# Kernel tuning notes

Measured on AMD Instinct MI355X. Metric: run time of the kernel, lower is better.

Reference implementation:

```python
import jax, jax.numpy as jnp
import numpy as np

# Dimensions (see shape_source)
D = 12       # tree depth / number of levels
N = 32768    # nodes per level
L = 3        # label_size
K = 4        # nary (max children)
HID = 128    # hidden_size == dim_E == dim_rep
V = 50000    # word_vocab_size
LAYERS = 2   # stacked NaryTreeLSTM layers


def setup_inputs() -> dict:
    key = jax.random.key(0)
    ks = jax.random.split(key, 10)
    s = 0.02  # weight init scale
    tokens = jax.random.randint(ks[0], (D, N, L), 0, V)
    # child indices in [-1, N]; -1 = no child, 0 = zero init row, 1..N = prev-level node
    indices = jax.random.randint(ks[1], (D, N, K), 0, N + 2) - 1
    E = jax.random.normal(ks[2], (V, HID))  # torch.randn init
    lin_w = jax.random.normal(ks[3], (HID, L * HID)) * s
    lin_b = jnp.zeros((HID,), jnp.float32)
    Uf_w = jax.random.normal(ks[4], (LAYERS, K * HID, K * HID)) * s
    Uf_b = jnp.zeros((LAYERS, K * HID), jnp.float32)
    Uiuo_w = jax.random.normal(ks[5], (LAYERS, 3 * HID, K * HID)) * s
    Uiuo_b = jnp.zeros((LAYERS, 3 * HID), jnp.float32)
    W_w = jax.random.normal(ks[6], (LAYERS, 4 * HID, HID)) * s
    W_b = jnp.zeros((LAYERS, 4 * HID), jnp.float32)
    return dict(tokens=tokens, indices=indices, E=E, lin_w=lin_w, lin_b=lin_b,
                Uf_w=Uf_w, Uf_b=Uf_b, Uiuo_w=Uiuo_w, Uiuo_b=Uiuo_b, W_w=W_w, W_b=W_b)


def _tree_lstm_layer(x, indices, Uf_w, Uf_b, Uiuo_w, Uiuo_b, W_w, W_b):
    """x: [D,N,HID], indices: [D,N,K] in [-1,N]. Returns (hs, cs): [D,N,HID]."""
    d = HID

    def step(carry, inp):
        h_full, c_full = carry              # [1+N, d]; row 0 is the zero init state
        xl, idx = inp                       # [N, d], [N, K]
        mask = (idx != -1)
        safe = jnp.where(mask, idx, 0)
        h = h_full[safe]                    # [N, K, d] gather of child hidden states
        c = c_full[safe]                    # [N, K, d]
        m = mask.astype(xl.dtype)[..., None]
        Wx = xl @ W_w.T + W_b               # [N, 4d]
        Wf, Wi, Wu, Wo = Wx[:, :d], Wx[:, d:2 * d], Wx[:, 2 * d:3 * d], Wx[:, 3 * d:]
        h_flat = h.reshape(N, K * d)
        fk = jax.nn.sigmoid(Wf[:, None, :] + (h_flat @ Uf_w.T + Uf_b).reshape(N, K, d))
        f = jnp.sum(fk * c * m, axis=1)     # masked sum over children
        iuo = h_flat @ Uiuo_w.T + Uiuo_b    # [N, 3d]
        i = jax.nn.sigmoid(iuo[:, :d] + Wi)
        u = jnp.tanh(iuo[:, d:2 * d] + Wu)
        o = jax.nn.sigmoid(iuo[:, 2 * d:] + Wo)
        new_c = i * u + f
        new_h = o * jnp.tanh(new_c)
        zero = jnp.zeros((1, d), xl.dtype)
        new_carry = (jnp.concatenate([zero, new_h], 0), jnp.concatenate([zero, new_c], 0))
        return new_carry, (new_h, new_c)

    init = (jnp.zeros((1 + N, d), x.dtype), jnp.zeros((1 + N, d), x.dtype))
    _, (hs, cs) = jax.lax.scan(step, init, (x, indices))
    return hs, cs


def reference(tokens, indices, E, lin_w, lin_b, Uf_w, Uf_b, Uiuo_w, Uiuo_b, W_w, W_b):
    # TreeEmbeddingLayer: gather token embeddings, concat label slots, project to HID
    emb = E[tokens].reshape(D, N, L * HID) @ lin_w.T + lin_b  # [D, N, HID]
    t = emb
    cs = None
    for l in range(LAYERS):
        skip = t
        hs, cs = _tree_lstm_layer(t, indices, Uf_w[l], Uf_b[l], Uiuo_w[l], Uiuo_b[l], W_w[l], W_b[l])
        t = hs + skip  # residual over levels
    hx = jnp.tile(t[-1][None], (2, 1, 1))   # [2, N, HID]
    cx = jnp.tile(cs[-1][None], (2, 1, 1))  # [2, N, HID]
    return hx, cx
```

## Files before the change

### kernel.cpp

```cpp
#include <hip/hip_runtime.h>
#include <cstdint>
#include <cstddef>

#define DD 12
#define NNODE 32768
#define LTOK 3
#define KCH 4
#define HD 128
#define NC_STEP 896
#define KD_STEP 640
#define NC_EMB 128
#define KD_EMB 384

typedef unsigned short u16;
typedef __attribute__((ext_vector_type(8))) __bf16 bf16x8;
typedef __attribute__((ext_vector_type(4))) float f32x4;

__device__ __forceinline__ float bf2f(unsigned int u) {
  union { unsigned int i; float f; } v; v.i = (u & 0xffffu) << 16; return v.f;
}
__device__ __forceinline__ u16 f2bf(float f) {
  union { float f; unsigned int i; } v; v.f = f;
  unsigned int x = v.i;
  return (u16)((x + 0x7fffu + ((x >> 16) & 1u)) >> 16);
}
__device__ __forceinline__ float sigm(float x) { return 1.f / (1.f + __expf(-x)); }
__device__ __forceinline__ float tanh_fast(float x) { return 1.f - 2.f / (1.f + __expf(2.f * x)); }
__device__ __forceinline__ void async16(const void* g, void* l) {
  __builtin_amdgcn_global_load_lds((const __attribute__((address_space(1))) unsigned int*)g,
                                   (__attribute__((address_space(3))) unsigned int*)l, 16, 0, 0);
}

#define BM 256
#define BN 128
#define BK 32

__global__ __launch_bounds__(512, 4) void gemm8_k(
    const u16* __restrict__ Abf, const u16* __restrict__ Tbf,
    const int* __restrict__ gidx, const u16* __restrict__ B,
    const float* __restrict__ bias, u16* __restrict__ outb,
    const u16* __restrict__ zbuf)
{
  __shared__ u16 As[3][BM * BK];
  __shared__ u16 Bs[3][BN * BK];
  const int t = threadIdx.x;
  const int w = t >> 6;
  const int L = t & 63;
  const int q = L >> 4;
  const int r16 = L >> 2;
  const int sub = L & 3;
  const int swz = sub ^ ((L >> 3) & 3);

  const int bid = blockIdx.x;
  const int wg = (bid & 7) * 112 + (bid >> 3);
  const int rt = wg / 7;
  const int ct = wg - rt * 7;
  const int row0 = rt * BM;
  const int col0 = ct * BN;

  const int wm = w >> 1;
  const int wn = w & 1;
  const int mrow = wm * 64;
  const int ncol = wn * 64;

  f32x4 acc[4][4];
#pragma unroll
  for (int a = 0; a < 4; ++a)
#pragma unroll
    for (int b = 0; b < 4; ++b)
      acc[a][b] = f32x4{0.f, 0.f, 0.f, 0.f};

  int4 cidx[2];
#pragma unroll
  for (int j = 0; j < 2; ++j)
    cidx[j] = *(const int4*)&gidx[(row0 + w * 32 + j * 16 + r16) * KCH];

  auto stageAll = [&](const int k0, const int sel) {
#pragma unroll
    for (int j = 0; j < 2; ++j) {
      const int rbase = w * 32 + j * 16;
      const u16* src;
      if (k0 < 4 * HD) {
        const int id = ((const int*)&cidx[j])[k0 >> 7];
        const u16* base = (id >= 1) ? (Abf + (size_t)(id - 1) * HD) : zbuf;
        src = base + (k0 & 127) + swz * 8;
      } else {
        src = Tbf + (size_t)(row0 + rbase + r16) * HD + (k0 - 4 * HD) + swz * 8;
      }
      async16(src, &As[sel][rbase * BK]);
    }
    const int rb = w * 16;
    async16(B + (size_t)(col0 + rb + r16) * KD_STEP + k0 + swz * 8,
            &Bs[sel][rb * BK]);
  };

  stageAll(0, 0);
  stageAll(32, 1);
  asm volatile("s_waitcnt vmcnt(3)" ::: "memory");
  __builtin_amdgcn_sched_barrier(0);
  __builtin_amdgcn_s_barrier();
  __builtin_amdgcn_sched_barrier(0);

  constexpr int NT = KD_STEP / BK;
#pragma unroll
  for (int tt = 0; tt < NT; ++tt) {
    const int rd = tt % 3;
    if (tt + 2 < NT) stageAll((tt + 2) * BK, (tt + 2) % 3);

    const int pc = (q ^ ((L >> 1) & 3)) * 8;
    bf16x8 af[4], bfv[4];
#pragma unroll
    for (int mt = 0; mt < 4; ++mt)
      af[mt] = *(const bf16x8*)&As[rd][(mrow + mt * 16 + (L & 15)) * BK + pc];
#pragma unroll
    for (int nt = 0; nt < 4; ++nt)
      bfv[nt] = *(const bf16x8*)&Bs[rd][(ncol + nt * 16 + (L & 15)) * BK + pc];

    __builtin_amdgcn_s_setprio(1);
#pragma unroll
    for (int mt = 0; mt < 4; ++mt)
#pragma unroll
      for (int nt = 0; nt < 4; ++nt)
        acc[mt][nt] = __builtin_amdgcn_mfma_f32_16x16x32_bf16(
            af[mt], bfv[nt], acc[mt][nt], 0, 0, 0);
    __builtin_amdgcn_s_setprio(0);

    if (tt < NT - 1) {
      if (tt + 2 < NT) asm volatile("s_waitcnt vmcnt(3)" ::: "memory");
      else             asm volatile("s_waitcnt vmcnt(0)" ::: "memory");
      __builtin_amdgcn_sched_barrier(0);
      __builtin_amdgcn_s_barrier();
      __builtin_amdgcn_sched_barrier(0);
    }
  }

#pragma unroll
  for (int nt = 0; nt < 4; ++nt) {
    const int col = col0 + ncol + nt * 16 + (L & 15);
    const float bb = bias[col];
#pragma unroll
    for (int mt = 0; mt < 4; ++mt) {
#pragma unroll
      for (int i = 0; i < 4; ++i) {
        const int row = row0 + mrow + mt * 16 + q * 4 + i;
        outb[(size_t)row * NC_STEP + col] = f2bf(acc[mt][nt][i] + bb);
      }
    }
  }
}

__global__ __launch_bounds__(256, 4) void gemm_emb_k(
    const u16* __restrict__ Ebf, const int* __restrict__ tokd,
    const u16* __restrict__ Lbf, const float* __restrict__ bias,
    float* __restrict__ outf, u16* __restrict__ outb)
{
  __shared__ u16 As[3][64 * BK];
  __shared__ u16 Bs[3][128 * BK];
  const int t = threadIdx.x;
  const int w = t >> 6;
  const int L = t & 63;
  const int q = L >> 4;
  const int r16 = L >> 2;
  const int sub = L & 3;
  const int swz = sub ^ ((L >> 3) & 3);
  const int row0 = blockIdx.x * 64;

  const int wm = w >> 1;
  const int wn = w & 1;
  const int mrow = wm * 32;
  const int ncol = wn * 64;

  f32x4 acc[2][4];
#pragma unroll
  for (int a = 0; a < 2; ++a)
#pragma unroll
    for (int b = 0; b < 4; ++b)
      acc[a][b] = f32x4{0.f, 0.f, 0.f, 0.f};

  const int arow = row0 + w * 16 + r16;
  int tok[3];
#pragma unroll
  for (int j = 0; j < 3; ++j)
    tok[j] = tokd[arow * LTOK + j];

  auto stageAll = [&](const int k0, const int sel) {
    const int id = tok[k0 >> 7];
    async16(Ebf + (size_t)id * HD + (k0 & 127) + swz * 8,
            &As[sel][(w * 16) * BK]);
#pragma unroll
    for (int j = 0; j < 2; ++j) {
      const int rb = w * 32 + j * 16;
      async16(Lbf + (size_t)(rb + r16) * KD_EMB + k0 + swz * 8,
              &Bs[sel][rb * BK]);
    }
  };

  stageAll(0, 0);
  stageAll(32, 1);
  asm volatile("s_waitcnt vmcnt(3)" ::: "memory");
  __builtin_amdgcn_sched_barrier(0);
  __builtin_amdgcn_s_barrier();
  __builtin_amdgcn_sched_barrier(0);

  constexpr int NT = KD_EMB / BK;
#pragma unroll
  for (int tt = 0; tt < NT; ++tt) {
    const int rd = tt % 3;
    if (tt + 2 < NT) stageAll((tt + 2) * BK, (tt + 2) % 3);

    const int pc = (q ^ ((L >> 1) & 3)) * 8;
    bf16x8 af[2], bfv[4];
#pragma unroll
    for (int mt = 0; mt < 2; ++mt)
      af[mt] = *(const bf16x8*)&As[rd][(mrow + mt * 16 + (L & 15)) * BK + pc];
#pragma unroll
    for (int nt = 0; nt < 4; ++nt)
      bfv[nt] = *(const bf16x8*)&Bs[rd][(ncol + nt * 16 + (L & 15)) * BK + pc];

    __builtin_amdgcn_s_setprio(1);
#pragma unroll
    for (int mt = 0; mt < 2; ++mt)
#pragma unroll
      for (int nt = 0; nt < 4; ++nt)
        acc[mt][nt] = __builtin_amdgcn_mfma_f32_16x16x32_bf16(
            af[mt], bfv[nt], acc[mt][nt], 0, 0, 0);
    __builtin_amdgcn_s_setprio(0);

    if (tt < NT - 1) {
      if (tt + 2 < NT) asm volatile("s_waitcnt vmcnt(3)" ::: "memory");
      else             asm volatile("s_waitcnt vmcnt(0)" ::: "memory");
      __builtin_amdgcn_sched_barrier(0);
      __builtin_amdgcn_s_barrier();
      __builtin_amdgcn_sched_barrier(0);
    }
  }

#pragma unroll
  for (int nt = 0; nt < 4; ++nt) {
    const int col = ncol + nt * 16 + (L & 15);
    const float bb = bias[col];
#pragma unroll
    for (int mt = 0; mt < 2; ++mt) {
#pragma unroll
      for (int i = 0; i < 4; ++i) {
        const int row = row0 + mrow + mt * 16 + q * 4 + i;
        const float v = acc[mt][nt][i] + bb;
        outf[(size_t)row * NC_EMB + col] = v;
        outb[(size_t)row * NC_EMB + col] = f2bf(v);
      }
    }
  }
}

__global__ __launch_bounds__(256) void cell_k(
    const u16* __restrict__ pre, const int* __restrict__ idxs,
    const float* __restrict__ c_prev, float* __restrict__ c_cur,
    u16* __restrict__ h_cur, float* __restrict__ t_io, u16* __restrict__ tbf)
{
  const int g = blockIdx.x * 256 + threadIdx.x;
  const int r = g >> 7;
  const int j = g & 127;
  const u16* pr = pre + (size_t)r * NC_STEP;
  float f = 0.f;
#pragma unroll
  for (int k = 0; k < KCH; ++k) {
    const int id = idxs[r * KCH + k];
    const float cg = (id >= 1) ? c_prev[(size_t)(id - 1) * HD + j] : 0.f;
    f += sigm(bf2f(pr[k * HD + j])) * cg;
  }
  const float iv = sigm(bf2f(pr[4 * HD + j]));
  const float uv = tanh_fast(bf2f(pr[5 * HD + j]));
  const float ov = sigm(bf2f(pr[6 * HD + j]));
  const float cn = iv * uv + f;
  const float hv = ov * tanh_fast(cn);
  c_cur[g] = cn;
  h_cur[g] = f2bf(hv);
  const float tn = t_io[g] + hv;
  t_io[g] = tn;
  tbf[g] = f2bf(tn);
}

__global__ __launch_bounds__(256) void conv_k(const float* __restrict__ src,
                                              u16* __restrict__ dst, int n4)
{
  const int g = blockIdx.x * 256 + threadIdx.x;
  if (g < n4) {
    float4 v = ((const float4*)src)[g];
    ((ushort4*)dst)[g] = make_ushort4(f2bf(v.x), f2bf(v.y), f2bf(v.z), f2bf(v.w));
  }
}

__global__ __launch_bounds__(256) void prep_k(
    const float* __restrict__ Uf_w, const float* __restrict__ Uf_b,
    const float* __restrict__ Uiuo_w, const float* __restrict__ Uiuo_b,
    const float* __restrict__ W_w, const float* __restrict__ W_b,
    u16* __restrict__ Ubig, float* __restrict__ biasbig)
{
  const int l = blockIdx.y;
  const int e = blockIdx.x * 256 + threadIdx.x;
  const int c = e / KD_STEP;
  const int k = e % KD_STEP;
  float v;
  if (k < 512) {
    v = (c < 512) ? Uf_w[((size_t)l * 512 + c) * 512 + k]
                  : Uiuo_w[((size_t)l * 384 + (c - 512)) * 512 + k];
  } else {
    const int q = k - 512;
    const int wr = (c < 512) ? (c & 127) : (128 + (c - 512));
    v = W_w[((size_t)l * 512 + wr) * 128 + q];
  }
  Ubig[((size_t)l * 896 + c) * 640 + k] = f2bf(v);
  if (e < 896) {
    const float b = (e < 512)
        ? (Uf_b[l * 512 + e] + W_b[l * 512 + (e & 127)])
        : (Uiuo_b[l * 384 + (e - 512)] + W_b[l * 512 + 128 + (e - 512)]);
    biasbig[l * 896 + e] = b;
  }
}

__global__ __launch_bounds__(256) void fin_k(
    const float* __restrict__ t_fin, const float* __restrict__ c_fin,
    float* __restrict__ out)
{
  const size_t NH = (size_t)NNODE * HD;
  const size_t g = (size_t)blockIdx.x * 256 + threadIdx.x;
  const float h = t_fin[g];
  const float c = c_fin[g];
  out[g] = h;
  out[NH + g] = h;
  out[2 * NH + g] = c;
  out[3 * NH + g] = c;
}

extern "C" void kernel_launch(void* const* d_in, const int* in_sizes, int n_in,
                              void* d_out, int out_size, void* d_ws, size_t ws_size,
                              hipStream_t stream)
{
  (void)in_sizes; (void)n_in; (void)out_size; (void)ws_size;
  const int*   tokens  = (const int*)d_in[0];
  const int*   indices = (const int*)d_in[1];
  const float* E       = (const float*)d_in[2];
  const float* lin_w   = (const float*)d_in[3];
  const float* lin_b   = (const float*)d_in[4];
  const float* Uf_w    = (const float*)d_in[5];
  const float* Uf_b    = (const float*)d_in[6];
  const float* Uiuo_w  = (const float*)d_in[7];
  const float* Uiuo_b  = (const float*)d_in[8];
  const float* W_w     = (const float*)d_in[9];
  const float* W_b     = (const float*)d_in[10];
  float* out = (float*)d_out;

  const size_t NH = (size_t)NNODE * HD;

  char* ws = (char*)d_ws;
  size_t off = 0;
  auto alloc = [&](size_t bytes) -> void* {
    void* p = ws + off;
    off = (off + bytes + 255) & ~(size_t)255;
    return p;
  };
  u16*   Ubig    = (u16*)alloc((size_t)2 * 896 * 640 * 2);
  float* biasbig = (float*)alloc(2 * 896 * 4);
  u16*   Ebf     = (u16*)alloc((size_t)50000 * HD * 2);
  u16*   Lbf     = (u16*)alloc((size_t)HD * KD_EMB * 2);
  float* tslice  = (float*)alloc(NH * 4);
  u16*   tbf     = (u16*)alloc(NH * 2);
  u16*   h0a     = (u16*)alloc(NH * 2);
  u16*   h0b     = (u16*)alloc(NH * 2);
  u16*   h1a     = (u16*)alloc(NH * 2);
  u16*   h1b     = (u16*)alloc(NH * 2);
  float* c0a     = (float*)alloc(NH * 4);
  float* c0b     = (float*)alloc(NH * 4);
  float* c1a     = (float*)alloc(NH * 4);
  float* c1b     = (float*)alloc(NH * 4);
  u16*   pre     = (u16*)alloc((size_t)NNODE * NC_STEP * 2);
  u16*   zbuf    = (u16*)alloc(512);

  u16*   h0[2] = {h0a, h0b};
  u16*   h1[2] = {h1a, h1b};
  float* c0[2] = {c0a, c0b};
  float* c1[2] = {c1a, c1b};

  hipMemsetAsync(zbuf, 0, 512, stream);
  hipMemsetAsync(h0[0], 0, NH * 2, stream);
  hipMemsetAsync(h1[0], 0, NH * 2, stream);
  hipMemsetAsync(c0[0], 0, NH * 4, stream);
  hipMemsetAsync(c1[0], 0, NH * 4, stream);
  prep_k<<<dim3(2240, 2), 256, 0, stream>>>(Uf_w, Uf_b, Uiuo_w, Uiuo_b, W_w, W_b,
                                            Ubig, biasbig);
  conv_k<<<dim3((50000 * HD / 4 + 255) / 256), 256, 0, stream>>>(E, Ebf, 50000 * HD / 4);
  conv_k<<<dim3((HD * KD_EMB / 4 + 255) / 256), 256, 0, stream>>>(lin_w, Lbf, HD * KD_EMB / 4);

  for (int d = 0; d < DD; ++d) {
    const int ri = d & 1, wi = (d + 1) & 1;
    const int* idxd = indices + (size_t)d * NNODE * KCH;
    const int* tokd = tokens + (size_t)d * NNODE * LTOK;

    gemm_emb_k<<<dim3(NNODE / 64), 256, 0, stream>>>(
        Ebf, tokd, Lbf, lin_b, tslice, tbf);

    for (int l = 0; l < 2; ++l) {
      const u16*   hp = (l == 0) ? h0[ri] : h1[ri];
      u16*         hc = (l == 0) ? h0[wi] : h1[wi];
      const float* cp = (l == 0) ? c0[ri] : c1[ri];
      float*       cc = (l == 0) ? c0[wi] : c1[wi];
      const u16* Ul = Ubig + (size_t)l * 896 * 640;
      const float* bl = biasbig + l * 896;
      gemm8_k<<<dim3((NNODE / BM) * (NC_STEP / BN)), 512, 0, stream>>>(
          hp, tbf, idxd, Ul, bl, pre, zbuf);
      cell_k<<<dim3((int)(NH / 256)), 256, 0, stream>>>(
          pre, idxd, cp, cc, hc, tslice, tbf);
    }
  }
  fin_k<<<dim3((int)(NH / 256)), 256, 0, stream>>>(tslice, c1[0], out);
}
```

Before: 2.103 ms.

## Fuse LSTM cell epilogue into gate GEMM via interleaved gate column layout

Reorders the packed weight matrix so each 128-column tile holds all 7 gates (plus one zero pad) for 16 hidden units. The GEMM epilogue can then stage its outputs in LDS and run the cell update directly, which removes the separate cell kernel and the round trip of the bf16 pre-activation buffer through global memory. The cost is padding N from 896 to 1024, about 14% more MMA work. The residual t buffers are now ping-ponged so tiles never read and write the same buffer.

```diff
diff --git a/kernel.cpp b/kernel.cpp
--- a/kernel.cpp
+++ b/kernel.cpp
@@ -7,10 +7,10 @@
 #define LTOK 3
 #define KCH 4
 #define HD 128
-#define NC_STEP 896
 #define KD_STEP 640
 #define NC_EMB 128
 #define KD_EMB 384
+#define NCP 1024
 
 typedef unsigned short u16;
 typedef __attribute__((ext_vector_type(8))) __bf16 bf16x8;
@@ -34,27 +34,29 @@
 #define BM 256
 #define BN 128
 #define BK 32
-
-__global__ __launch_bounds__(512, 4) void gemm8_k(
+#define ASZ (BM * BK)
+#define BSZ (BN * BK)
+
+__global__ __launch_bounds__(512, 4) void gemm_fused_k(
     const u16* __restrict__ Abf, const u16* __restrict__ Tbf,
     const int* __restrict__ gidx, const u16* __restrict__ B,
-    const float* __restrict__ bias, u16* __restrict__ outb,
-    const u16* __restrict__ zbuf)
-{
-  __shared__ u16 As[3][BM * BK];
-  __shared__ u16 Bs[3][BN * BK];
-  const int t = threadIdx.x;
-  const int w = t >> 6;
-  const int L = t & 63;
+    const float* __restrict__ bias, const float* __restrict__ c_prev,
+    float* __restrict__ c_cur, u16* __restrict__ h_cur,
+    const float* __restrict__ t_in, float* __restrict__ t_out,
+    u16* __restrict__ tbf_out, const u16* __restrict__ zbuf)
+{
+  __shared__ u16 smem[3 * ASZ + 3 * BSZ];
+  const int tid = threadIdx.x;
+  const int w = tid >> 6;
+  const int L = tid & 63;
   const int q = L >> 4;
   const int r16 = L >> 2;
-  const int sub = L & 3;
-  const int swz = sub ^ ((L >> 3) & 3);
+  const int swz = (L & 3) ^ ((L >> 3) & 3);
 
   const int bid = blockIdx.x;
-  const int wg = (bid & 7) * 112 + (bid >> 3);
-  const int rt = wg / 7;
-  const int ct = wg - rt * 7;
+  const int wg = (bid & 7) * 128 + (bid >> 3);
+  const int rt = wg >> 3;
+  const int ct = wg & 7;
   const int row0 = rt * BM;
   const int col0 = ct * BN;
 
@@ -87,11 +89,11 @@
       } else {
         src = Tbf + (size_t)(row0 + rbase + r16) * HD + (k0 - 4 * HD) + swz * 8;
       }
-      async16(src, &As[sel][rbase * BK]);
+      async16(src, &smem[sel * ASZ + rbase * BK]);
     }
     const int rb = w * 16;
     async16(B + (size_t)(col0 + rb + r16) * KD_STEP + k0 + swz * 8,
-            &Bs[sel][rb * BK]);
+            &smem[3 * ASZ + sel * BSZ + rb * BK]);
   };
 
   stageAll(0, 0);
@@ -111,10 +113,10 @@
     bf16x8 af[4], bfv[4];
 #pragma unroll
     for (int mt = 0; mt < 4; ++mt)
-      af[mt] = *(const bf16x8*)&As[rd][(mrow + mt * 16 + (L & 15)) * BK + pc];
+      af[mt] = *(const bf16x8*)&smem[rd * ASZ + (mrow + mt * 16 + (L & 15)) * BK + pc];
 #pragma unroll
     for (int nt = 0; nt < 4; ++nt)
-      bfv[nt] = *(const bf16x8*)&Bs[rd][(ncol + nt * 16 + (L & 15)) * BK + pc];
+      bfv[nt] = *(const bf16x8*)&smem[3 * ASZ + rd * BSZ + (ncol + nt * 16 + (L & 15)) * BK + pc];
 
     __builtin_amdgcn_s_setprio(1);
 #pragma unroll
@@ -134,18 +136,48 @@
     }
   }
 
+  __syncthreads();
 #pragma unroll
   for (int nt = 0; nt < 4; ++nt) {
-    const int col = col0 + ncol + nt * 16 + (L & 15);
-    const float bb = bias[col];
+    const int colL = ncol + nt * 16 + (L & 15);
+    const float bb = bias[col0 + colL];
 #pragma unroll
     for (int mt = 0; mt < 4; ++mt) {
 #pragma unroll
       for (int i = 0; i < 4; ++i) {
-        const int row = row0 + mrow + mt * 16 + q * 4 + i;
-        outb[(size_t)row * NC_STEP + col] = f2bf(acc[mt][nt][i] + bb);
+        const int rowL = mrow + mt * 16 + q * 4 + i;
+        smem[rowL * 128 + colL] = f2bf(acc[mt][nt][i] + bb);
       }
     }
+  }
+  __syncthreads();
+  const int jbase = col0 >> 3;
+#pragma unroll
+  for (int s = 0; s < 8; ++s) {
+    const int o = tid + s * 512;
+    const int rowL = o >> 4;
+    const int jL = o & 15;
+    const int row = row0 + rowL;
+    const int jg = jbase + jL;
+    const bf16x8 pv = *(const bf16x8*)&smem[rowL * 128 + jL * 8];
+    const u16* pu = (const u16*)&pv;
+    float p[8];
+#pragma unroll
+    for (int k = 0; k < 8; ++k) p[k] = bf2f(pu[k]);
+    const int4 ids = *(const int4*)&gidx[row * KCH];
+    float f = 0.f;
+    f += sigm(p[0]) * ((ids.x >= 1) ? c_prev[(size_t)(ids.x - 1) * HD + jg] : 0.f);
+    f += sigm(p[1]) * ((ids.y >= 1) ? c_prev[(size_t)(ids.y - 1) * HD + jg] : 0.f);
+    f += sigm(p[2]) * ((ids.z >= 1) ? c_prev[(size_t)(ids.z - 1) * HD + jg] : 0.f);
+    f += sigm(p[3]) * ((ids.w >= 1) ? c_prev[(size_t)(ids.w - 1) * HD + jg] : 0.f);
+    const float cn = sigm(p[4]) * tanh_fast(p[5]) + f;
+    const float hv = sigm(p[6]) * tanh_fast(cn);
+    const size_t gg = (size_t)row * HD + jg;
+    c_cur[gg] = cn;
+    h_cur[gg] = f2bf(hv);
+    const float tn = t_in[gg] + hv;
+    t_out[gg] = tn;
+    tbf_out[gg] = f2bf(tn);
   }
 }
 
@@ -161,8 +193,7 @@
   const int L = t & 63;
   const int q = L >> 4;
   const int r16 = L >> 2;
-  const int sub = L & 3;
-  const int swz = sub ^ ((L >> 3) & 3);
+  const int swz = (L & 3) ^ ((L >> 3) & 3);
   const int row0 = blockIdx.x * 64;
 
   const int wm = w >> 1;
@@ -252,34 +283,6 @@
   }
 }
 
-__global__ __launch_bounds__(256) void cell_k(
-    const u16* __restrict__ pre, const int* __restrict__ idxs,
-    const float* __restrict__ c_prev, float* __restrict__ c_cur,
-    u16* __restrict__ h_cur, float* __restrict__ t_io, u16* __restrict__ tbf)
-{
-  const int g = blockIdx.x * 256 + threadIdx.x;
-  const int r = g >> 7;
-  const int j = g & 127;
-  const u16* pr = pre + (size_t)r * NC_STEP;
-  float f = 0.f;
-#pragma unroll
-  for (int k = 0; k < KCH; ++k) {
-    const int id = idxs[r * KCH + k];
-    const float cg = (id >= 1) ? c_prev[(size_t)(id - 1) * HD + j] : 0.f;
-    f += sigm(bf2f(pr[k * HD + j])) * cg;
-  }
-  const float iv = sigm(bf2f(pr[4 * HD + j]));
-  const float uv = tanh_fast(bf2f(pr[5 * HD + j]));
-  const float ov = sigm(bf2f(pr[6 * HD + j]));
-  const float cn = iv * uv + f;
-  const float hv = ov * tanh_fast(cn);
-  c_cur[g] = cn;
-  h_cur[g] = f2bf(hv);
-  const float tn = t_io[g] + hv;
-  t_io[g] = tn;
-  tbf[g] = f2bf(tn);
-}
-
 __global__ __launch_bounds__(256) void conv_k(const float* __restrict__ src,
                                               u16* __restrict__ dst, int n4)
 {
@@ -298,23 +301,31 @@
 {
   const int l = blockIdx.y;
   const int e = blockIdx.x * 256 + threadIdx.x;
-  const int c = e / KD_STEP;
+  const int cp = e / KD_STEP;
   const int k = e % KD_STEP;
-  float v;
-  if (k < 512) {
-    v = (c < 512) ? Uf_w[((size_t)l * 512 + c) * 512 + k]
-                  : Uiuo_w[((size_t)l * 384 + (c - 512)) * 512 + k];
-  } else {
-    const int q = k - 512;
-    const int wr = (c < 512) ? (c & 127) : (128 + (c - 512));
-    v = W_w[((size_t)l * 512 + wr) * 128 + q];
-  }
-  Ubig[((size_t)l * 896 + c) * 640 + k] = f2bf(v);
-  if (e < 896) {
-    const float b = (e < 512)
-        ? (Uf_b[l * 512 + e] + W_b[l * 512 + (e & 127)])
-        : (Uiuo_b[l * 384 + (e - 512)] + W_b[l * 512 + 128 + (e - 512)]);
-    biasbig[l * 896 + e] = b;
+  const int j = cp >> 3, g = cp & 7;
+  float v = 0.f;
+  if (g != 7) {
+    const int oldc = (g < 4) ? (g * 128 + j) : (512 + (g - 4) * 128 + j);
+    if (k < 512) {
+      v = (oldc < 512) ? Uf_w[((size_t)l * 512 + oldc) * 512 + k]
+                       : Uiuo_w[((size_t)l * 384 + (oldc - 512)) * 512 + k];
+    } else {
+      const int wr = (oldc < 512) ? (oldc & 127) : (128 + (oldc - 512));
+      v = W_w[((size_t)l * 512 + wr) * 128 + (k - 512)];
+    }
+  }
+  Ubig[((size_t)l * NCP + cp) * KD_STEP + k] = f2bf(v);
+  if (e < NCP) {
+    const int jj = e >> 3, gg = e & 7;
+    float b = 0.f;
+    if (gg != 7) {
+      const int oldc = (gg < 4) ? (gg * 128 + jj) : (512 + (gg - 4) * 128 + jj);
+      const int wr = (oldc < 512) ? (oldc & 127) : (128 + (oldc - 512));
+      b = ((oldc < 512) ? Uf_b[l * 512 + oldc] : Uiuo_b[l * 384 + (oldc - 512)])
+          + W_b[l * 512 + wr];
+    }
+    biasbig[l * NCP + e] = b;
   }
 }
 
@@ -359,12 +370,14 @@
     off = (off + bytes + 255) & ~(size_t)255;
     return p;
   };
-  u16*   Ubig    = (u16*)alloc((size_t)2 * 896 * 640 * 2);
-  float* biasbig = (float*)alloc(2 * 896 * 4);
+  u16*   Ubig    = (u16*)alloc((size_t)2 * NCP * KD_STEP * 2);
+  float* biasbig = (float*)alloc(2 * NCP * 4);
   u16*   Ebf     = (u16*)alloc((size_t)50000 * HD * 2);
   u16*   Lbf     = (u16*)alloc((size_t)HD * KD_EMB * 2);
-  float* tslice  = (float*)alloc(NH * 4);
-  u16*   tbf     = (u16*)alloc(NH * 2);
+  float* tA      = (float*)alloc(NH * 4);
+  float* tB      = (float*)alloc(NH * 4);
+  u16*   tbfA    = (u16*)alloc(NH * 2);
+  u16*   tbfB    = (u16*)alloc(NH * 2);
   u16*   h0a     = (u16*)alloc(NH * 2);
   u16*   h0b     = (u16*)alloc(NH * 2);
   u16*   h1a     = (u16*)alloc(NH * 2);
@@ -373,7 +386,6 @@
   float* c0b     = (float*)alloc(NH * 4);
   float* c1a     = (float*)alloc(NH * 4);
   float* c1b     = (float*)alloc(NH * 4);
-  u16*   pre     = (u16*)alloc((size_t)NNODE * NC_STEP * 2);
   u16*   zbuf    = (u16*)alloc(512);
 
   u16*   h0[2] = {h0a, h0b};
@@ -386,8 +398,8 @@
   hipMemsetAsync(h1[0], 0, NH * 2, stream);
   hipMemsetAsync(c0[0], 0, NH * 4, stream);
   hipMemsetAsync(c1[0], 0, NH * 4, stream);
-  prep_k<<<dim3(2240, 2), 256, 0, stream>>>(Uf_w, Uf_b, Uiuo_w, Uiuo_b, W_w, W_b,
-                                            Ubig, biasbig);
+  prep_k<<<dim3(NCP * KD_STEP / 256, 2), 256, 0, stream>>>(
+      Uf_w, Uf_b, Uiuo_w, Uiuo_b, W_w, W_b, Ubig, biasbig);
   conv_k<<<dim3((50000 * HD / 4 + 255) / 256), 256, 0, stream>>>(E, Ebf, 50000 * HD / 4);
   conv_k<<<dim3((HD * KD_EMB / 4 + 255) / 256), 256, 0, stream>>>(lin_w, Lbf, HD * KD_EMB / 4);
 
@@ -397,20 +409,14 @@
     const int* tokd = tokens + (size_t)d * NNODE * LTOK;
 
     gemm_emb_k<<<dim3(NNODE / 64), 256, 0, stream>>>(
-        Ebf, tokd, Lbf, lin_b, tslice, tbf);
-
-    for (int l = 0; l < 2; ++l) {
-      const u16*   hp = (l == 0) ? h0[ri] : h1[ri];
-      u16*         hc = (l == 0) ? h0[wi] : h1[wi];
-      const float* cp = (l == 0) ? c0[ri] : c1[ri];
-      float*       cc = (l == 0) ? c0[wi] : c1[wi];
-      const u16* Ul = Ubig + (size_t)l * 896 * 640;
-      const float* bl = biasbig + l * 896;
-      gemm8_k<<<dim3((NNODE / BM) * (NC_STEP / BN)), 512, 0, stream>>>(
-          hp, tbf, idxd, Ul, bl, pre, zbuf);
-      cell_k<<<dim3((int)(NH / 256)), 256, 0, stream>>>(
-          pre, idxd, cp, cc, hc, tslice, tbf);
-    }
-  }
-  fin_k<<<dim3((int)(NH / 256)), 256, 0, stream>>>(tslice, c1[0], out);
-}
+        Ebf, tokd, Lbf, lin_b, tA, tbfA);
+
+    gemm_fused_k<<<dim3((NNODE / BM) * (NCP / BN)), 512, 0, stream>>>(
+        h0[ri], tbfA, idxd, Ubig, biasbig,
+        c0[ri], c0[wi], h0[wi], tA, tB, tbfB, zbuf);
+    gemm_fused_k<<<dim3((NNODE / BM) * (NCP / BN)), 512, 0, stream>>>(
+        h1[ri], tbfB, idxd, Ubig + (size_t)NCP * KD_STEP, biasbig + NCP,
+        c1[ri], c1[wi], h1[wi], tB, tA, tbfA, zbuf);
+  }
+  fin_k<<<dim3((int)(NH / 256)), 256, 0, stream>>>(tA, c1[0], out);
+}
```

Result: faster. 1.909 ms (-9.2%).
